# Kernel tuning notes

Hardware: AMD Instinct MI355X
Metric: run time of the kernel (lower is better)

The kernel has to match this reference:

```python
import jax, jax.numpy as jnp
import numpy as np

E, D_IN, H, D_OUT = 8, 6, 32, 2
B = 1048576

def setup_inputs() -> dict:
    key = jax.random.key(0)
    ks = jax.random.split(key, 11)
    s = lambda *sh: 1.0 / np.sqrt(sh[-2])  # glorot-ish scale
    x = jax.random.normal(ks[0], (B, D_IN), dtype=jnp.float32)
    # stacked expert weights
    W1 = jax.random.normal(ks[1], (E, D_IN, H), dtype=jnp.float32) * (1.0/np.sqrt(D_IN))
    b1 = jnp.zeros((E, H), dtype=jnp.float32)
    W2 = jax.random.normal(ks[2], (E, H, H), dtype=jnp.float32) * (1.0/np.sqrt(H))
    b2 = jnp.zeros((E, H), dtype=jnp.float32)
    W3 = jax.random.normal(ks[3], (E, H, D_OUT), dtype=jnp.float32) * (1.0/np.sqrt(H))
    b3 = jnp.zeros((E, D_OUT), dtype=jnp.float32)
    # gating network
    Wg1 = jax.random.normal(ks[4], (D_IN, H), dtype=jnp.float32) * (1.0/np.sqrt(D_IN))
    bg1 = jnp.zeros((H,), dtype=jnp.float32)
    Wg2 = jax.random.normal(ks[5], (H, E), dtype=jnp.float32) * (1.0/np.sqrt(H))
    bg2 = jnp.zeros((E,), dtype=jnp.float32)
    return {"x": x, "W1": W1, "b1": b1, "W2": W2, "b2": b2, "W3": W3, "b3": b3,
            "Wg1": Wg1, "bg1": bg1, "Wg2": Wg2, "bg2": bg2}

def reference(x, W1, b1, W2, b2, W3, b3, Wg1, bg1, Wg2, bg2):
    # gate: [B, E] softmax probs
    g = jax.nn.softmax(jax.nn.relu(x @ Wg1 + bg1) @ Wg2 + bg2, axis=-1)
    # all experts as batched GEMMs: h1, h2 [B, E, H]; y [B, E, 2]
    h1 = jax.nn.relu(jnp.einsum('bd,edh->beh', x, W1) + b1)
    h2 = jax.nn.relu(jnp.einsum('beh,ehk->bek', h1, W2) + b2)
    y = jnp.einsum('beh,eho->beo', h2, W3) + b3
    # gate-weighted sum over experts -> [B, 2]
    return jnp.einsum('be,beo->bo', g, y)
```

## Files before the change

kernel.cpp:

```cpp
#include <hip/hip_runtime.h>


typedef _Float16 half2_t __attribute__((ext_vector_type(2)));
typedef _Float16 half4_t __attribute__((ext_vector_type(4)));
typedef _Float16 half8_t __attribute__((ext_vector_type(8)));
typedef __fp16   fp16v2  __attribute__((ext_vector_type(2)));
typedef float  float4_t __attribute__((ext_vector_type(4)));
typedef float  float2_t __attribute__((ext_vector_type(2)));
typedef int    int2_t   __attribute__((ext_vector_type(2)));
typedef int    int4_t   __attribute__((ext_vector_type(4)));

#define MFMA_K32(A, B, C) __builtin_amdgcn_mfma_f32_16x16x32_f16((A), (B), (C), 0, 0, 0)
#define MFMA_K16(A, B, C) __builtin_amdgcn_mfma_f32_16x16x16f16((A), (B), (C), 0, 0, 0)

static constexpr int E_ = 8, DIN_ = 6, H_ = 32, TB_ = 4;

union H8U { half2_t h2[4]; half8_t h8; int4_t i4; };
union H4U { half2_t h2[2]; half4_t h4; int2_t i2; };
union W1U { H4U f[2]; int4_t i4; };
union HI  { half2_t h; int i; };
union PKU { fp16v2 p; half2_t h; };

__device__ __forceinline__ half2_t pkrtz(float a, float b) {
    PKU u; u.p = __builtin_amdgcn_cvt_pkrtz(a, b);
    return u.h;
}

__device__ __forceinline__ half2_t relu2(half2_t v) {
    const half2_t z = {(_Float16)0.0f, (_Float16)0.0f};
    return __builtin_elementwise_max(v, z);
}

__device__ __forceinline__ void gate_eval(
    half4_t xB, const H4U* G1, const H8U& G2, float4_t bg2F, float4_t zero4,
    int gsrc, int q, float& ga, float& gb, float& rs)
{
    float4_t hgLo = MFMA_K16(G1[0].h4, xB, zero4);
    float4_t hgHi = MFMA_K16(G1[1].h4, xB, zero4);
    H8U uh;
    uh.h2[0] = relu2(pkrtz(hgLo[0], hgLo[1]));
    uh.h2[1] = relu2(pkrtz(hgLo[2], hgLo[3]));
    uh.h2[2] = relu2(pkrtz(hgHi[0], hgHi[1]));
    uh.h2[3] = relu2(pkrtz(hgHi[2], hgHi[3]));
    float4_t gl = MFMA_K32(G2.h8, uh.h8, bg2F);
    float ex0 = __builtin_amdgcn_exp2f(gl[0]);
    float ex1 = __builtin_amdgcn_exp2f(gl[1]);
    float ex2 = __builtin_amdgcn_exp2f(gl[2]);
    float ex3 = __builtin_amdgcn_exp2f(gl[3]);
    float s = (ex0 + ex1) + (ex2 + ex3);
    s += __shfl_xor(s, 16);
    rs = __builtin_amdgcn_rcpf(s);
    HI pa, pb;
    pa.h = pkrtz(ex0, ex1);
    pb.h = pkrtz(ex2, ex3);
    int va = __builtin_amdgcn_ds_bpermute(gsrc, pa.i);
    int vb = __builtin_amdgcn_ds_bpermute(gsrc, pb.i);
    HI gsel; gsel.i = (q & 1) ? vb : va;
    ga = (float)gsel.h[0];
    gb = (float)gsel.h[1];
}

__global__ __launch_bounds__(256)
__attribute__((amdgpu_waves_per_eu(2, 2)))
void moe_kernel(
    const float* __restrict__ x,  const float* __restrict__ W1, const float* __restrict__ b1,
    const float* __restrict__ W2, const float* __restrict__ b2, const float* __restrict__ W3,
    const float* __restrict__ b3, const float* __restrict__ Wg1, const float* __restrict__ bg1,
    const float* __restrict__ Wg2, const float* __restrict__ bg2,
    float* __restrict__ out, int nTiles, int tilesPerWave)
{
    const int tid  = threadIdx.x;
    const int lane = tid & 63;
    const int t    = lane & 15;
    const int q    = lane >> 4;
    const int wv   = tid >> 6;
    const int gw   = (blockIdx.x << 2) + wv;
    const int eo   = t >> 1;

    __shared__ W1U w1img[E_][64];
    __shared__ H8U w2img[E_][2][64];
    __shared__ H8U b2img[E_][64];

    const float L2E = 1.44269504f;

    #pragma unroll
    for (int j = 0; j < 2; ++j) {
        const int e = wv * 2 + j;
        W1U w1v;
        #pragma unroll
        for (int f = 0; f < 2; ++f) {
            float v0 = 0.f, v1 = 0.f, v2 = 0.f, v3 = 0.f;
            const float* We = W1 + (size_t)e * DIN_ * H_ + f * 16 + t;
            if (q == 0)      { v0 = We[0 * H_]; v1 = We[1 * H_]; v2 = We[2 * H_]; v3 = We[3 * H_]; }
            else if (q == 1) { v0 = We[4 * H_]; v1 = We[5 * H_]; v2 = b1[e * H_ + f * 16 + t]; }
            w1v.f[f].h2[0] = pkrtz(v0, v1); w1v.f[f].h2[1] = pkrtz(v2, v3);
        }
        w1img[e][lane] = w1v;
        H8U w2lo, w2hi, b2v;
        #pragma unroll
        for (int p = 0; p < 4; ++p) {
            int c0 = ((p >> 1) << 4) + q * 4 + ((p & 1) << 1);
            w2lo.h2[p] = pkrtz(W2[(e * H_ + c0) * H_ + 0  + t], W2[(e * H_ + c0 + 1) * H_ + 0  + t]);
            w2hi.h2[p] = pkrtz(W2[(e * H_ + c0) * H_ + 16 + t], W2[(e * H_ + c0 + 1) * H_ + 16 + t]);
            b2v.h2[p]  = pkrtz(b2[e * H_ + c0], b2[e * H_ + c0 + 1]);
        }
        w2img[e][0][lane] = w2lo;
        w2img[e][1][lane] = w2hi;
        b2img[e][lane]    = b2v;
    }

    H4U G1[2];
    #pragma unroll
    for (int f = 0; f < 2; ++f) {
        float v0 = 0.f, v1 = 0.f, v2 = 0.f, v3 = 0.f;
        if (q == 0) {
            v0 = Wg1[0 * H_ + f * 16 + t]; v1 = Wg1[1 * H_ + f * 16 + t];
            v2 = Wg1[2 * H_ + f * 16 + t]; v3 = Wg1[3 * H_ + f * 16 + t];
        } else if (q == 1) {
            v0 = Wg1[4 * H_ + f * 16 + t]; v1 = Wg1[5 * H_ + f * 16 + t];
            v2 = bg1[f * 16 + t];          v3 = 0.f;
        }
        G1[f].h2[0] = pkrtz(v0, v1); G1[f].h2[1] = pkrtz(v2, v3);
    }
    H8U G2;
    #pragma unroll
    for (int p = 0; p < 4; ++p) {
        int c0 = ((p >> 1) << 4) + q * 4 + ((p & 1) << 1);
        float v0 = (t < E_) ? Wg2[c0 * E_ + t] * L2E : 0.f;
        float v1 = (t < E_) ? Wg2[(c0 + 1) * E_ + t] * L2E : 0.f;
        G2.h2[p] = pkrtz(v0, v1);
    }

    H8U W3S;
    #pragma unroll
    for (int p = 0; p < 4; ++p) {
        int c0 = ((p >> 1) << 4) + q * 4 + ((p & 1) << 1);
        W3S.h2[p] = pkrtz(W3[(eo * H_ + c0) * 2 + (t & 1)], W3[(eo * H_ + c0 + 1) * 2 + (t & 1)]);
    }

    float4_t bg2F, b3F;
    #pragma unroll
    for (int r = 0; r < 4; ++r) {
        int m = q * 4 + r;
        bg2F[r] = (m < E_) ? bg2[m] * L2E : 0.f;
        b3F[r]  = b3[m];
    }
    const float4_t zero4 = {0.f, 0.f, 0.f, 0.f};
    const int4_t  zeroi  = {0, 0, 0, 0};

    const int gsrc = ((((q >> 1) << 4) | t) << 2);

    __syncthreads();

    const int tile0 = gw * tilesPerWave;

    const int xo1 = (q == 0) ? 0 : 4;
    const int xo2 = (q == 0) ? 2 : 4;
    const float* xq = x + ((size_t)tile0 * 16 + t) * DIN_;
    float2_t la[TB_], lb[TB_];
    #pragma unroll
    for (int u = 0; u < TB_; ++u) {
        la[u] = float2_t{0.f, 0.f};
        lb[u] = float2_t{0.f, 0.f};
        if (tile0 + u < nTiles) {
            la[u] = *(const float2_t*)(xq + (size_t)u * 16 * DIN_ + xo1);
            lb[u] = *(const float2_t*)(xq + (size_t)u * 16 * DIN_ + xo2);
        }
    }

    HI onei; onei.h = pkrtz(1.f, 0.f);
    const bool isq0 = (q == 0);

    for (int it = 0; it < tilesPerWave; it += TB_) {
        const int tb = tile0 + it;
        if (tb >= nTiles) break;

        H4U ux[TB_];
        #pragma unroll
        for (int u = 0; u < TB_; ++u) {
            ux[u].h2[0] = pkrtz(la[u][0], la[u][1]);
            HI hb; hb.h = pkrtz(lb[u][0], lb[u][1]);
            HI se; se.i = isq0 ? hb.i : onei.i;
            ux[u].h2[1] = se.h;
        }

        if (it + TB_ < tilesPerWave) {
            const float* xn = xq + (size_t)(it + TB_) * 16 * DIN_;
            #pragma unroll
            for (int u = 0; u < TB_; ++u) {
                if (tb + TB_ + u < nTiles) {
                    la[u] = *(const float2_t*)(xn + (size_t)u * 16 * DIN_ + xo1);
                    lb[u] = *(const float2_t*)(xn + (size_t)u * 16 * DIN_ + xo2);
                }
            }
        }

        float ga[TB_], gb[TB_], rs[TB_];
        #pragma unroll
        for (int u = 0; u < TB_; ++u)
            gate_eval(ux[u].h4, G1, G2, bg2F, zero4, gsrc, q, ga[u], gb[u], rs[u]);

        float4_t Ya[TB_], Yb[TB_];
        #pragma unroll
        for (int u = 0; u < TB_; ++u) { Ya[u] = b3F; Yb[u] = zero4; }
        #pragma unroll
        for (int e = 0; e < E_; ++e) {
            W1U w1v  = w1img[e][lane];
            H8U w2lo = w2img[e][0][lane];
            H8U w2hi = w2img[e][1][lane];
            H8U b2v  = b2img[e][lane];
            H8U a3;  a3.i4 = (eo == e) ? W3S.i4 : zeroi;

            #pragma unroll
            for (int u = 0; u < TB_; ++u) {
                float4_t lo = MFMA_K16(w1v.f[0].h4, ux[u].h4, zero4);
                float4_t hi = MFMA_K16(w1v.f[1].h4, ux[u].h4, zero4);
                H8U u1;
                u1.h2[0] = relu2(pkrtz(lo[0], lo[1]));
                u1.h2[1] = relu2(pkrtz(lo[2], lo[3]));
                u1.h2[2] = relu2(pkrtz(hi[0], hi[1]));
                u1.h2[3] = relu2(pkrtz(hi[2], hi[3]));
                float4_t lo2 = MFMA_K32(w2lo.h8, u1.h8, zero4);
                float4_t hi2 = MFMA_K32(w2hi.h8, u1.h8, zero4);
                H8U u2;
                u2.h2[0] = relu2(pkrtz(lo2[0], lo2[1]) + b2v.h2[0]);
                u2.h2[1] = relu2(pkrtz(lo2[2], lo2[3]) + b2v.h2[1]);
                u2.h2[2] = relu2(pkrtz(hi2[0], hi2[1]) + b2v.h2[2]);
                u2.h2[3] = relu2(pkrtz(hi2[2], hi2[3]) + b2v.h2[3]);
                if (e & 1) Yb[u] = MFMA_K32(a3.h8, u2.h8, Yb[u]);
                else       Ya[u] = MFMA_K32(a3.h8, u2.h8, Ya[u]);
            }
        }

        #pragma unroll
        for (int u = 0; u < TB_; ++u) {
            const int tile = tb + u;
            float p0 = ga[u] * (Ya[u][0] + Yb[u][0]) + gb[u] * (Ya[u][2] + Yb[u][2]);
            float p1 = ga[u] * (Ya[u][1] + Yb[u][1]) + gb[u] * (Ya[u][3] + Yb[u][3]);
            p0 += __shfl_xor(p0, 16);
            p0 += __shfl_xor(p0, 32);
            p1 += __shfl_xor(p1, 16);
            p1 += __shfl_xor(p1, 32);
            if (tile < nTiles && lane < 16) {
                float2_t o = {p0 * rs[u], p1 * rs[u]};
                *(float2_t*)(out + ((size_t)tile * 16 + t) * 2) = o;
            }
        }
    }
}

extern "C" void kernel_launch(void* const* d_in, const int* in_sizes, int n_in,
                              void* d_out, int out_size, void* d_ws, size_t ws_size,
                              hipStream_t stream) {
    const float* x   = (const float*)d_in[0];
    const float* W1  = (const float*)d_in[1];
    const float* b1  = (const float*)d_in[2];
    const float* W2  = (const float*)d_in[3];
    const float* b2  = (const float*)d_in[4];
    const float* W3  = (const float*)d_in[5];
    const float* b3  = (const float*)d_in[6];
    const float* Wg1 = (const float*)d_in[7];
    const float* bg1 = (const float*)d_in[8];
    const float* Wg2 = (const float*)d_in[9];
    const float* bg2 = (const float*)d_in[10];
    float* out = (float*)d_out;

    const int B      = in_sizes[0] / DIN_;
    const int nTiles = (B + 15) / 16;
    const int blocks = 512;
    const int wavesTotal = blocks * 4;
    const int tpw = (nTiles + wavesTotal - 1) / wavesTotal;

    moe_kernel<<<blocks, 256, 0, stream>>>(x, W1, b1, W2, b2, W3, b3,
                                           Wg1, bg1, Wg2, bg2, out, nTiles, tpw);
}
```

Before: 134.5 us.

## Raise occupancy by moving gate/W3 weights to LDS and folding b2 into MFMA

Measured after the change: 129.2 us. -3.9%, faster.

```diff
diff --git a/kernel.cpp b/kernel.cpp
--- a/kernel.cpp
+++ b/kernel.cpp
@@ -13,7 +13,7 @@
 #define MFMA_K32(A, B, C) __builtin_amdgcn_mfma_f32_16x16x32_f16((A), (B), (C), 0, 0, 0)
 #define MFMA_K16(A, B, C) __builtin_amdgcn_mfma_f32_16x16x16f16((A), (B), (C), 0, 0, 0)
 
-static constexpr int E_ = 8, DIN_ = 6, H_ = 32, TB_ = 4;
+static constexpr int E_ = 8, DIN_ = 6, H_ = 32, TB_ = 2;
 
 union H8U { half2_t h2[4]; half8_t h8; int4_t i4; };
 union H4U { half2_t h2[2]; half4_t h4; int2_t i2; };
@@ -61,7 +61,7 @@
 }
 
 __global__ __launch_bounds__(256)
-__attribute__((amdgpu_waves_per_eu(2, 2)))
+__attribute__((amdgpu_waves_per_eu(3, 3)))
 void moe_kernel(
     const float* __restrict__ x,  const float* __restrict__ W1, const float* __restrict__ b1,
     const float* __restrict__ W2, const float* __restrict__ b2, const float* __restrict__ W3,
@@ -77,9 +77,12 @@
     const int gw   = (blockIdx.x << 2) + wv;
     const int eo   = t >> 1;
 
-    __shared__ W1U w1img[E_][64];
-    __shared__ H8U w2img[E_][2][64];
-    __shared__ H8U b2img[E_][64];
+    __shared__ W1U  w1img[E_][64];
+    __shared__ H8U  w2img[E_][2][64];
+    __shared__ float b2f32[E_][H_];
+    __shared__ W1U  g1img[64];
+    __shared__ H8U  g2img[64];
+    __shared__ H8U  w3img[64];
 
     const float L2E = 1.44269504f;
 
@@ -96,46 +99,45 @@
             w1v.f[f].h2[0] = pkrtz(v0, v1); w1v.f[f].h2[1] = pkrtz(v2, v3);
         }
         w1img[e][lane] = w1v;
-        H8U w2lo, w2hi, b2v;
+        H8U w2lo, w2hi;
         #pragma unroll
         for (int p = 0; p < 4; ++p) {
             int c0 = ((p >> 1) << 4) + q * 4 + ((p & 1) << 1);
             w2lo.h2[p] = pkrtz(W2[(e * H_ + c0) * H_ + 0  + t], W2[(e * H_ + c0 + 1) * H_ + 0  + t]);
             w2hi.h2[p] = pkrtz(W2[(e * H_ + c0) * H_ + 16 + t], W2[(e * H_ + c0 + 1) * H_ + 16 + t]);
-            b2v.h2[p]  = pkrtz(b2[e * H_ + c0], b2[e * H_ + c0 + 1]);
         }
         w2img[e][0][lane] = w2lo;
         w2img[e][1][lane] = w2hi;
-        b2img[e][lane]    = b2v;
-    }
-
-    H4U G1[2];
-    #pragma unroll
-    for (int f = 0; f < 2; ++f) {
-        float v0 = 0.f, v1 = 0.f, v2 = 0.f, v3 = 0.f;
-        if (q == 0) {
-            v0 = Wg1[0 * H_ + f * 16 + t]; v1 = Wg1[1 * H_ + f * 16 + t];
-            v2 = Wg1[2 * H_ + f * 16 + t]; v3 = Wg1[3 * H_ + f * 16 + t];
-        } else if (q == 1) {
-            v0 = Wg1[4 * H_ + f * 16 + t]; v1 = Wg1[5 * H_ + f * 16 + t];
-            v2 = bg1[f * 16 + t];          v3 = 0.f;
-        }
-        G1[f].h2[0] = pkrtz(v0, v1); G1[f].h2[1] = pkrtz(v2, v3);
-    }
-    H8U G2;
-    #pragma unroll
-    for (int p = 0; p < 4; ++p) {
-        int c0 = ((p >> 1) << 4) + q * 4 + ((p & 1) << 1);
-        float v0 = (t < E_) ? Wg2[c0 * E_ + t] * L2E : 0.f;
-        float v1 = (t < E_) ? Wg2[(c0 + 1) * E_ + t] * L2E : 0.f;
-        G2.h2[p] = pkrtz(v0, v1);
-    }
-
-    H8U W3S;
-    #pragma unroll
-    for (int p = 0; p < 4; ++p) {
-        int c0 = ((p >> 1) << 4) + q * 4 + ((p & 1) << 1);
-        W3S.h2[p] = pkrtz(W3[(eo * H_ + c0) * 2 + (t & 1)], W3[(eo * H_ + c0 + 1) * 2 + (t & 1)]);
+        if (lane < H_) b2f32[e][lane] = b2[e * H_ + lane];
+    }
+
+    if (wv == 0) {
+        W1U g1v;
+        #pragma unroll
+        for (int f = 0; f < 2; ++f) {
+            float v0 = 0.f, v1 = 0.f, v2 = 0.f, v3 = 0.f;
+            if (q == 0) {
+                v0 = Wg1[0 * H_ + f * 16 + t]; v1 = Wg1[1 * H_ + f * 16 + t];
+                v2 = Wg1[2 * H_ + f * 16 + t]; v3 = Wg1[3 * H_ + f * 16 + t];
+            } else if (q == 1) {
+                v0 = Wg1[4 * H_ + f * 16 + t]; v1 = Wg1[5 * H_ + f * 16 + t];
+                v2 = bg1[f * 16 + t];          v3 = 0.f;
+            }
+            g1v.f[f].h2[0] = pkrtz(v0, v1); g1v.f[f].h2[1] = pkrtz(v2, v3);
+        }
+        g1img[lane] = g1v;
+        H8U g2v, w3v;
+        #pragma unroll
+        for (int p = 0; p < 4; ++p) {
+            int c0 = ((p >> 1) << 4) + q * 4 + ((p & 1) << 1);
+            float v0 = (t < E_) ? Wg2[c0 * E_ + t] * L2E : 0.f;
+            float v1 = (t < E_) ? Wg2[(c0 + 1) * E_ + t] * L2E : 0.f;
+            g2v.h2[p] = pkrtz(v0, v1);
+            w3v.h2[p] = pkrtz(W3[(eo * H_ + c0) * 2 + (t & 1)],
+                              W3[(eo * H_ + c0 + 1) * 2 + (t & 1)]);
+        }
+        g2img[lane] = g2v;
+        w3img[lane] = w3v;
     }
 
     float4_t bg2F, b3F;
@@ -175,6 +177,10 @@
         const int tb = tile0 + it;
         if (tb >= nTiles) break;
 
+        W1U g1v; g1v.i4 = *(const volatile int4_t*)&g1img[lane].i4;
+        H8U g2v; g2v.i4 = *(const volatile int4_t*)&g2img[lane].i4;
+        H8U w3v; w3v.i4 = *(const volatile int4_t*)&w3img[lane].i4;
+
         H4U ux[TB_];
         #pragma unroll
         for (int u = 0; u < TB_; ++u) {
@@ -198,7 +204,7 @@
         float ga[TB_], gb[TB_], rs[TB_];
         #pragma unroll
         for (int u = 0; u < TB_; ++u)
-            gate_eval(ux[u].h4, G1, G2, bg2F, zero4, gsrc, q, ga[u], gb[u], rs[u]);
+            gate_eval(ux[u].h4, g1v.f, g2v, bg2F, zero4, gsrc, q, ga[u], gb[u], rs[u]);
 
         float4_t Ya[TB_], Yb[TB_];
         #pragma unroll
@@ -208,8 +214,9 @@
             W1U w1v  = w1img[e][lane];
             H8U w2lo = w2img[e][0][lane];
             H8U w2hi = w2img[e][1][lane];
-            H8U b2v  = b2img[e][lane];
-            H8U a3;  a3.i4 = (eo == e) ? W3S.i4 : zeroi;
+            float4_t b2clo = *(const float4_t*)&b2f32[e][q * 4];
+            float4_t b2chi = *(const float4_t*)&b2f32[e][16 + q * 4];
+            H8U a3;  a3.i4 = (eo == e) ? w3v.i4 : zeroi;
 
             #pragma unroll
             for (int u = 0; u < TB_; ++u) {
@@ -220,13 +227,13 @@
                 u1.h2[1] = relu2(pkrtz(lo[2], lo[3]));
                 u1.h2[2] = relu2(pkrtz(hi[0], hi[1]));
                 u1.h2[3] = relu2(pkrtz(hi[2], hi[3]));
-                float4_t lo2 = MFMA_K32(w2lo.h8, u1.h8, zero4);
-                float4_t hi2 = MFMA_K32(w2hi.h8, u1.h8, zero4);
+                float4_t lo2 = MFMA_K32(w2lo.h8, u1.h8, b2clo);
+                float4_t hi2 = MFMA_K32(w2hi.h8, u1.h8, b2chi);
                 H8U u2;
-                u2.h2[0] = relu2(pkrtz(lo2[0], lo2[1]) + b2v.h2[0]);
-                u2.h2[1] = relu2(pkrtz(lo2[2], lo2[3]) + b2v.h2[1]);
-                u2.h2[2] = relu2(pkrtz(hi2[0], hi2[1]) + b2v.h2[2]);
-                u2.h2[3] = relu2(pkrtz(hi2[2], hi2[3]) + b2v.h2[3]);
+                u2.h2[0] = relu2(pkrtz(lo2[0], lo2[1]));
+                u2.h2[1] = relu2(pkrtz(lo2[2], lo2[3]));
+                u2.h2[2] = relu2(pkrtz(hi2[0], hi2[1]));
+                u2.h2[3] = relu2(pkrtz(hi2[2], hi2[3]));
                 if (e & 1) Yb[u] = MFMA_K32(a3.h8, u2.h8, Yb[u]);
                 else       Ya[u] = MFMA_K32(a3.h8, u2.h8, Ya[u]);
             }
@@ -267,7 +274,7 @@
 
     const int B      = in_sizes[0] / DIN_;
     const int nTiles = (B + 15) / 16;
-    const int blocks = 512;
+    const int blocks = 768;
     const int wavesTotal = blocks * 4;
     const int tpw = (nTiles + wavesTotal - 1) / wavesTotal;
 
```
